# Optimization experiments

Hardware: AMD Instinct MI355X
Metric: run time of the kernel (lower is better)

Reference implementation:

```python
import jax, jax.numpy as jnp
import numpy as np

EPS = 1e-3  # matches MaskedBatchNorm2d default eps=0.001


def setup_inputs() -> dict:
    key = jax.random.key(0)
    k1, k2 = jax.random.split(key)
    B, C, W, H = 16, 64, 256, 256
    x = jax.random.normal(k1, (B, C, W, H), dtype=jnp.float32)
    # densified sparse-voxel feature maps the module is designed for.
    keep = (jax.random.uniform(k2, (B, W, H)) < 0.3).astype(jnp.float32)
    x = x * keep[:, None, :, :]
    return {"x": x}


def reference(x):
    """Faithful masked batchnorm (training mode, affine=False).

    Original: per-batch nonzero() of channel-sum, pad index lists to the max
    count with zeros (i.e. duplicate location (0,0)), gather [B, Nmax, C],
    compute per-channel mean/var over ALL gathered entries (padding included),
    divide by sqrt(var+eps) (mean NOT subtracted in output), scatter back to
    nonzero locations — padded rows also overwrite location (0,0).
    """
    B, C, W, H = x.shape
    x1 = x.sum(axis=1)                      # [B, W, H]
    m = x1 != 0                             # nonzero-site mask
    mf = m.astype(x.dtype)
    n = mf.sum(axis=(1, 2))                 # nonzero count per batch item [B]
    Nmax = n.max()
    pad = Nmax - n                          # number of padded (0,0) duplicates per item
    total = (B * Nmax).astype(x.dtype)      # B * max(num_nonzeros)

    x00 = x[:, :, 0, 0]                     # [B, C] value gathered by padded indices

    # per-channel mean over masked sites + padded duplicates of (0,0)
    sum_c = jnp.einsum('bcwh,bwh->c', x, mf) + jnp.einsum('bc,b->c', x00, pad)
    mean = sum_c / total                    # [C]

    d = x - mean[None, :, None, None]
    var = (jnp.einsum('bcwh,bwh->c', d * d, mf)
           + jnp.einsum('bc,b->c', (x00 - mean[None, :]) ** 2, pad)) / total

    inv = 1.0 / jnp.sqrt(var + EPS)         # [C]; note: mean is NOT subtracted
    xn = x * inv[None, :, None, None]

    out = jnp.where(m[:, None, :, :], xn, x)
    # padded scatter rows write normalized x[b,:,0,0] into location (0,0)
    has_pad = (pad > 0)[:, None]            # [B,1]
    out = out.at[:, :, 0, 0].set(jnp.where(has_pad, x00 * inv[None, :], out[:, :, 0, 0]))
    return out
```

## Files before the change

kernel.cpp:

```cpp
#include <hip/hip_runtime.h>


#define NB 16
#define CB 64
#define WH 65536
#define TILE 256
#define NTILES (NB * WH / TILE)
#define GRID1 1024
#define TPT (NTILES / GRID1)
#define DIRTY_CAP 512
#define EPS 0.001f


__global__ __launch_bounds__(256, 4)
void mbn_pass1(const float* __restrict__ x, float* __restrict__ sqPart,
               unsigned* __restrict__ nPart, unsigned* __restrict__ dirtyCnt,
               int* __restrict__ dirtyLoc) {
    __shared__ float lds_s[4][TILE];
    __shared__ float lds_a[4][TILE];
    __shared__ unsigned cnt_lds[16];
    const int tid  = threadIdx.x;
    const int wave = tid >> 6;
    const int lane = tid & 63;
    if (tid < 16) cnt_lds[tid] = 0;

    float sAcc[16], qAcc[16];
#pragma unroll
    for (int j = 0; j < 16; ++j) { sAcc[j] = 0.f; qAcc[j] = 0.f; }
    __syncthreads();

    for (int tt = 0; tt < TPT; ++tt) {
        const int tile = blockIdx.x + tt * GRID1;
        const int b    = tile >> 8;
        const int whb  = (tile & 255) * TILE;
        const float* base = x + (((size_t)(b * 64 + wave * 16)) << 16) + whb + lane * 4;

        float sp0 = 0.f, sp1 = 0.f, sp2 = 0.f, sp3 = 0.f;
        float aa0 = 0.f, aa1 = 0.f, aa2 = 0.f, aa3 = 0.f;
#pragma unroll
        for (int j = 0; j < 16; ++j) {
            float4 v = *(const float4*)(base + ((size_t)j << 16));
            sp0 += v.x; sp1 += v.y; sp2 += v.z; sp3 += v.w;
            aa0 += fabsf(v.x); aa1 += fabsf(v.y); aa2 += fabsf(v.z); aa3 += fabsf(v.w);
            sAcc[j] += (v.x + v.y) + (v.z + v.w);
            qAcc[j] = fmaf(v.x, v.x, qAcc[j]);
            qAcc[j] = fmaf(v.y, v.y, qAcc[j]);
            qAcc[j] = fmaf(v.z, v.z, qAcc[j]);
            qAcc[j] = fmaf(v.w, v.w, qAcc[j]);
        }
        *(float4*)&lds_s[wave][lane * 4] = make_float4(sp0, sp1, sp2, sp3);
        *(float4*)&lds_a[wave][lane * 4] = make_float4(aa0, aa1, aa2, aa3);
        __syncthreads();

        float s = lds_s[0][tid] + lds_s[1][tid] + lds_s[2][tid] + lds_s[3][tid];
        float a = lds_a[0][tid] + lds_a[1][tid] + lds_a[2][tid] + lds_a[3][tid];
        bool mask = (s != 0.0f);
        unsigned long long bal = __ballot(mask);
        if (lane == 0) atomicAdd(&cnt_lds[b], (unsigned)__popcll(bal));
        if (!mask && a != 0.0f) {
            unsigned idx = atomicAdd(dirtyCnt, 1u);
            if (idx < DIRTY_CAP) dirtyLoc[idx] = (b << 16) | (whb + tid);
        }
        __syncthreads();
    }

#pragma unroll
    for (int j = 0; j < 16; ++j) {
        float sv = sAcc[j], qv = qAcc[j];
        for (int off = 32; off; off >>= 1) {
            sv += __shfl_xor(sv, off);
            qv += __shfl_xor(qv, off);
        }
        if (lane == 0) {
            sqPart[blockIdx.x * 128 + wave * 16 + j]      = sv;
            sqPart[blockIdx.x * 128 + 64 + wave * 16 + j] = qv;
        }
    }
    __syncthreads();
    if (tid < 16) nPart[blockIdx.x * 16 + tid] = cnt_lds[tid];
}

__global__ void mbn_finalize(const float* __restrict__ x, const float* __restrict__ sqPart,
                             const unsigned* __restrict__ nPart,
                             const unsigned* __restrict__ dirtyCnt, const int* __restrict__ dirtyLoc,
                             float* __restrict__ inv, int* __restrict__ padOut) {
    __shared__ float red[256];
    __shared__ float sq[128];
    __shared__ unsigned npar[4][16];
    __shared__ unsigned ntot[16];
    const int t = threadIdx.x;
    const int idx = t & 127, half = t >> 7;

    float acc = 0.f;
    const float* p = sqPart + (size_t)half * 512 * 128 + idx;
#pragma unroll 8
    for (int blk = 0; blk < 512; ++blk) acc += p[(size_t)blk * 128];
    red[t] = acc;

    if (t >= 192) {
        const int b = t & 15, q = (t >> 4) & 3;
        unsigned s = 0;
        const unsigned* np = nPart + q * 256 * 16 + b;
#pragma unroll 8
        for (int blk = 0; blk < 256; ++blk) s += np[blk * 16];
        npar[q][b] = s;
    }
    __syncthreads();
    if (t < 128) sq[t] = red[t] + red[t + 128];
    if (t < 16)  ntot[t] = npar[0][t] + npar[1][t] + npar[2][t] + npar[3][t];
    __syncthreads();

    if (t < 64) {
        const int c = t;
        unsigned nmax = 0;
#pragma unroll
        for (int b = 0; b < NB; ++b) { unsigned nb = ntot[b]; nmax = nb > nmax ? nb : nmax; }
        const float total = (float)(16u * nmax);

        float s = sq[c], q = sq[64 + c];
        unsigned cnt = *dirtyCnt; if (cnt > DIRTY_CAP) cnt = DIRTY_CAP;
        for (unsigned i = 0; i < cnt; ++i) {
            int loc = dirtyLoc[i];
            int b = loc >> 16, wh = loc & 65535;
            float v = x[(((size_t)(b * 64 + c)) << 16) + wh];
            s -= v; q -= v * v;
        }
        float p1 = 0.f, p2 = 0.f;
#pragma unroll
        for (int b = 0; b < NB; ++b) {
            float padf = (float)(nmax - ntot[b]);
            float v00  = x[((size_t)(b * 64 + c)) << 16];
            p1 = fmaf(padf, v00, p1);
            p2 = fmaf(padf, v00 * v00, p2);
            if (c == 0) padOut[b] = (int)(nmax - ntot[b]);
        }
        float mean = (s + p1) / total;
        float var  = (q + p2) / total - mean * mean;
        inv[c] = 1.0f / sqrtf(var + EPS);
    }
}

__global__ __launch_bounds__(256)
void mbn_pass2(const float4* __restrict__ x4, float4* __restrict__ out4,
               const float* __restrict__ inv) {
    const int blk = blockIdx.x;
    const float sc = inv[(blk >> 3) & 63];
    const size_t base = (size_t)blk * 2048 + threadIdx.x;
#pragma unroll
    for (int k = 0; k < 8; ++k) {
        size_t i = base + (size_t)k * 256;
        float4 v = x4[i];
        v.x *= sc; v.y *= sc; v.z *= sc; v.w *= sc;
        out4[i] = v;
    }
}

__global__ void mbn_fixup(const float* __restrict__ x, float* __restrict__ out,
                          const unsigned* __restrict__ dirtyCnt, const int* __restrict__ dirtyLoc,
                          const int* __restrict__ padArr) {
    const int c = threadIdx.x;
    unsigned cnt = *dirtyCnt; if (cnt > DIRTY_CAP) cnt = DIRTY_CAP;
    for (unsigned i = 0; i < cnt; ++i) {
        int loc = dirtyLoc[i];
        int b = loc >> 16, wh = loc & 65535;
        if (wh == 0 && padArr[b] > 0) continue;
        size_t idx = (((size_t)(b * 64 + c)) << 16) + wh;
        out[idx] = x[idx];
    }
}

extern "C" void kernel_launch(void* const* d_in, const int* in_sizes, int n_in,
                              void* d_out, int out_size, void* d_ws, size_t ws_size,
                              hipStream_t stream) {
    const float* x = (const float*)d_in[0];
    float* out = (float*)d_out;
    float* wsf = (float*)d_ws;

    float*    sqPart   = wsf;
    unsigned* nPart    = (unsigned*)(wsf + 131072);
    unsigned* dirtyCnt = (unsigned*)(wsf + 147456);
    float*    inv      = wsf + 147520;
    int*      padArr   = (int*)(wsf + 147584);
    int*      dirtyLoc = (int*)(wsf + 147600);

    hipMemsetAsync((char*)d_ws + 147456 * 4, 0, 64, stream);

    mbn_pass1<<<GRID1, 256, 0, stream>>>(x, sqPart, nPart, dirtyCnt, dirtyLoc);
    mbn_finalize<<<1, 256, 0, stream>>>(x, sqPart, nPart, dirtyCnt, dirtyLoc, inv, padArr);
    mbn_pass2<<<8192, 256, 0, stream>>>((const float4*)x, (float4*)out, inv);
    mbn_fixup<<<1, 64, 0, stream>>>(x, out, dirtyCnt, dirtyLoc, padArr);
}
```

Measured before the change: 592.4 us.

## Restructure stats pass to contiguous per-block tiles, widen finalize, nontemporal scale stores

```diff
diff --git a/kernel.cpp b/kernel.cpp
--- a/kernel.cpp
+++ b/kernel.cpp
@@ -2,112 +2,132 @@
 
 
 #define NB 16
-#define CB 64
-#define WH 65536
-#define TILE 256
-#define NTILES (NB * WH / TILE)
-#define GRID1 1024
-#define TPT (NTILES / GRID1)
 #define DIRTY_CAP 512
 #define EPS 0.001f
+#define GRID1 1024
+
+typedef float vfloat4 __attribute__((ext_vector_type(4)));
 
 
 __global__ __launch_bounds__(256, 4)
 void mbn_pass1(const float* __restrict__ x, float* __restrict__ sqPart,
                unsigned* __restrict__ nPart, unsigned* __restrict__ dirtyCnt,
                int* __restrict__ dirtyLoc) {
-    __shared__ float lds_s[4][TILE];
-    __shared__ float lds_a[4][TILE];
-    __shared__ unsigned cnt_lds[16];
+    __shared__ float lds_s[4][1024];
+    __shared__ float lds_a[4][1024];
+    __shared__ unsigned cntw[4];
+
     const int tid  = threadIdx.x;
     const int wave = tid >> 6;
     const int lane = tid & 63;
-    if (tid < 16) cnt_lds[tid] = 0;
+    const int blk  = blockIdx.x;
+    const int b    = blk >> 6;
+    const int whb0 = (blk & 63) << 10;
 
     float sAcc[16], qAcc[16];
 #pragma unroll
     for (int j = 0; j < 16; ++j) { sAcc[j] = 0.f; qAcc[j] = 0.f; }
-    __syncthreads();
-
-    for (int tt = 0; tt < TPT; ++tt) {
-        const int tile = blockIdx.x + tt * GRID1;
-        const int b    = tile >> 8;
-        const int whb  = (tile & 255) * TILE;
-        const float* base = x + (((size_t)(b * 64 + wave * 16)) << 16) + whb + lane * 4;
-
-        float sp0 = 0.f, sp1 = 0.f, sp2 = 0.f, sp3 = 0.f;
-        float aa0 = 0.f, aa1 = 0.f, aa2 = 0.f, aa3 = 0.f;
-#pragma unroll
-        for (int j = 0; j < 16; ++j) {
-            float4 v = *(const float4*)(base + ((size_t)j << 16));
-            sp0 += v.x; sp1 += v.y; sp2 += v.z; sp3 += v.w;
-            aa0 += fabsf(v.x); aa1 += fabsf(v.y); aa2 += fabsf(v.z); aa3 += fabsf(v.w);
-            sAcc[j] += (v.x + v.y) + (v.z + v.w);
-            qAcc[j] = fmaf(v.x, v.x, qAcc[j]);
-            qAcc[j] = fmaf(v.y, v.y, qAcc[j]);
-            qAcc[j] = fmaf(v.z, v.z, qAcc[j]);
-            qAcc[j] = fmaf(v.w, v.w, qAcc[j]);
-        }
-        *(float4*)&lds_s[wave][lane * 4] = make_float4(sp0, sp1, sp2, sp3);
-        *(float4*)&lds_a[wave][lane * 4] = make_float4(aa0, aa1, aa2, aa3);
-        __syncthreads();
-
-        float s = lds_s[0][tid] + lds_s[1][tid] + lds_s[2][tid] + lds_s[3][tid];
-        float a = lds_a[0][tid] + lds_a[1][tid] + lds_a[2][tid] + lds_a[3][tid];
-        bool mask = (s != 0.0f);
-        unsigned long long bal = __ballot(mask);
-        if (lane == 0) atomicAdd(&cnt_lds[b], (unsigned)__popcll(bal));
-        if (!mask && a != 0.0f) {
-            unsigned idx = atomicAdd(dirtyCnt, 1u);
-            if (idx < DIRTY_CAP) dirtyLoc[idx] = (b << 16) | (whb + tid);
-        }
-        __syncthreads();
-    }
+
+    const float* wbase = x + (((size_t)(b * 64 + wave * 16)) << 16) + whb0 + lane * 4;
+
+#pragma unroll
+    for (int j = 0; j < 4; ++j) {
+        const float* cb = wbase + j * 256;
+        float4 sp = make_float4(0.f, 0.f, 0.f, 0.f);
+        float4 aa = make_float4(0.f, 0.f, 0.f, 0.f);
+#pragma unroll
+        for (int c = 0; c < 16; ++c) {
+            float4 v = *(const float4*)(cb + ((size_t)c << 16));
+            sp.x += v.x; sp.y += v.y; sp.z += v.z; sp.w += v.w;
+            aa.x += fabsf(v.x); aa.y += fabsf(v.y); aa.z += fabsf(v.z); aa.w += fabsf(v.w);
+            sAcc[c] += (v.x + v.y) + (v.z + v.w);
+            qAcc[c] = fmaf(v.x, v.x, qAcc[c]);
+            qAcc[c] = fmaf(v.y, v.y, qAcc[c]);
+            qAcc[c] = fmaf(v.z, v.z, qAcc[c]);
+            qAcc[c] = fmaf(v.w, v.w, qAcc[c]);
+        }
+        *(float4*)&lds_s[wave][j * 256 + lane * 4] = sp;
+        *(float4*)&lds_a[wave][j * 256 + lane * 4] = aa;
+    }
+    __syncthreads();
+
+    float4 s0 = *(const float4*)&lds_s[0][tid * 4];
+    float4 s1 = *(const float4*)&lds_s[1][tid * 4];
+    float4 s2 = *(const float4*)&lds_s[2][tid * 4];
+    float4 s3 = *(const float4*)&lds_s[3][tid * 4];
+    float4 a0 = *(const float4*)&lds_a[0][tid * 4];
+    float4 a1 = *(const float4*)&lds_a[1][tid * 4];
+    float4 a2 = *(const float4*)&lds_a[2][tid * 4];
+    float4 a3 = *(const float4*)&lds_a[3][tid * 4];
+    float sx = (s0.x + s1.x) + (s2.x + s3.x);
+    float sy = (s0.y + s1.y) + (s2.y + s3.y);
+    float sz = (s0.z + s1.z) + (s2.z + s3.z);
+    float sw = (s0.w + s1.w) + (s2.w + s3.w);
+    float ax = (a0.x + a1.x) + (a2.x + a3.x);
+    float ay = (a0.y + a1.y) + (a2.y + a3.y);
+    float az = (a0.z + a1.z) + (a2.z + a3.z);
+    float aw = (a0.w + a1.w) + (a2.w + a3.w);
+    bool m0 = (sx != 0.f), m1 = (sy != 0.f), m2 = (sz != 0.f), m3 = (sw != 0.f);
+    unsigned cnt = (m0 ? 1u : 0u) + (m1 ? 1u : 0u) + (m2 ? 1u : 0u) + (m3 ? 1u : 0u);
+    if ((!m0 && ax != 0.f) | (!m1 && ay != 0.f) | (!m2 && az != 0.f) | (!m3 && aw != 0.f)) {
+        bool d[4] = { !m0 && ax != 0.f, !m1 && ay != 0.f, !m2 && az != 0.f, !m3 && aw != 0.f };
+        for (int k = 0; k < 4; ++k) if (d[k]) {
+            unsigned id = atomicAdd(dirtyCnt, 1u);
+            if (id < DIRTY_CAP) dirtyLoc[id] = (b << 16) | (whb0 + tid * 4 + k);
+        }
+    }
+#pragma unroll
+    for (int off = 32; off; off >>= 1) cnt += __shfl_xor(cnt, off);
+    if (lane == 0) cntw[wave] = cnt;
 
 #pragma unroll
     for (int j = 0; j < 16; ++j) {
         float sv = sAcc[j], qv = qAcc[j];
+#pragma unroll
         for (int off = 32; off; off >>= 1) {
             sv += __shfl_xor(sv, off);
             qv += __shfl_xor(qv, off);
         }
         if (lane == 0) {
-            sqPart[blockIdx.x * 128 + wave * 16 + j]      = sv;
-            sqPart[blockIdx.x * 128 + 64 + wave * 16 + j] = qv;
-        }
-    }
-    __syncthreads();
-    if (tid < 16) nPart[blockIdx.x * 16 + tid] = cnt_lds[tid];
-}
-
-__global__ void mbn_finalize(const float* __restrict__ x, const float* __restrict__ sqPart,
-                             const unsigned* __restrict__ nPart,
-                             const unsigned* __restrict__ dirtyCnt, const int* __restrict__ dirtyLoc,
-                             float* __restrict__ inv, int* __restrict__ padOut) {
-    __shared__ float red[256];
+            sqPart[blk * 128 + wave * 16 + j]      = sv;
+            sqPart[blk * 128 + 64 + wave * 16 + j] = qv;
+        }
+    }
+    __syncthreads();
+    if (tid == 0) nPart[blk] = cntw[0] + cntw[1] + cntw[2] + cntw[3];
+}
+
+__global__ __launch_bounds__(1024)
+void mbn_finalize(const float* __restrict__ x, const float* __restrict__ sqPart,
+                  const unsigned* __restrict__ nPart,
+                  const unsigned* __restrict__ dirtyCnt, const int* __restrict__ dirtyLoc,
+                  float* __restrict__ inv, int* __restrict__ padOut) {
+    __shared__ float red[1024];
     __shared__ float sq[128];
-    __shared__ unsigned npar[4][16];
     __shared__ unsigned ntot[16];
     const int t = threadIdx.x;
-    const int idx = t & 127, half = t >> 7;
+    const int col = t & 127, grp = t >> 7;
 
     float acc = 0.f;
-    const float* p = sqPart + (size_t)half * 512 * 128 + idx;
+    const float* p = sqPart + (size_t)grp * 128 * 128 + col;
 #pragma unroll 8
-    for (int blk = 0; blk < 512; ++blk) acc += p[(size_t)blk * 128];
+    for (int r = 0; r < 128; ++r) acc += p[(size_t)r * 128];
     red[t] = acc;
 
-    if (t >= 192) {
-        const int b = t & 15, q = (t >> 4) & 3;
+    if (t < 16) {
         unsigned s = 0;
-        const unsigned* np = nPart + q * 256 * 16 + b;
+        const unsigned* np = nPart + t * 64;
 #pragma unroll 8
-        for (int blk = 0; blk < 256; ++blk) s += np[blk * 16];
-        npar[q][b] = s;
-    }
-    __syncthreads();
-    if (t < 128) sq[t] = red[t] + red[t + 128];
-    if (t < 16)  ntot[t] = npar[0][t] + npar[1][t] + npar[2][t] + npar[3][t];
+        for (int i = 0; i < 64; ++i) s += np[i];
+        ntot[t] = s;
+    }
+    __syncthreads();
+    if (t < 128) {
+        float v = 0.f;
+#pragma unroll
+        for (int g = 0; g < 8; ++g) v += red[g * 128 + t];
+        sq[t] = v;
+    }
     __syncthreads();
 
     if (t < 64) {
@@ -141,17 +161,17 @@
 }
 
 __global__ __launch_bounds__(256)
-void mbn_pass2(const float4* __restrict__ x4, float4* __restrict__ out4,
+void mbn_pass2(const vfloat4* __restrict__ x4, vfloat4* __restrict__ out4,
                const float* __restrict__ inv) {
     const int blk = blockIdx.x;
-    const float sc = inv[(blk >> 3) & 63];
-    const size_t base = (size_t)blk * 2048 + threadIdx.x;
-#pragma unroll
-    for (int k = 0; k < 8; ++k) {
+    const float sc = inv[(blk >> 2) & 63];
+    const size_t base = ((size_t)blk << 12) + threadIdx.x;
+#pragma unroll
+    for (int k = 0; k < 16; ++k) {
         size_t i = base + (size_t)k * 256;
-        float4 v = x4[i];
-        v.x *= sc; v.y *= sc; v.z *= sc; v.w *= sc;
-        out4[i] = v;
+        vfloat4 v = x4[i];
+        v *= sc;
+        __builtin_nontemporal_store(v, &out4[i]);
     }
 }
 
@@ -178,15 +198,15 @@
 
     float*    sqPart   = wsf;
     unsigned* nPart    = (unsigned*)(wsf + 131072);
-    unsigned* dirtyCnt = (unsigned*)(wsf + 147456);
-    float*    inv      = wsf + 147520;
-    int*      padArr   = (int*)(wsf + 147584);
-    int*      dirtyLoc = (int*)(wsf + 147600);
-
-    hipMemsetAsync((char*)d_ws + 147456 * 4, 0, 64, stream);
+    unsigned* dirtyCnt = (unsigned*)(wsf + 132160);
+    float*    inv      = wsf + 132224;
+    int*      padArr   = (int*)(wsf + 132288);
+    int*      dirtyLoc = (int*)(wsf + 132352);
+
+    (void)hipMemsetAsync((char*)d_ws + 132160 * 4, 0, 64, stream);
 
     mbn_pass1<<<GRID1, 256, 0, stream>>>(x, sqPart, nPart, dirtyCnt, dirtyLoc);
-    mbn_finalize<<<1, 256, 0, stream>>>(x, sqPart, nPart, dirtyCnt, dirtyLoc, inv, padArr);
-    mbn_pass2<<<8192, 256, 0, stream>>>((const float4*)x, (float4*)out, inv);
+    mbn_finalize<<<1, 1024, 0, stream>>>(x, sqPart, nPart, dirtyCnt, dirtyLoc, inv, padArr);
+    mbn_pass2<<<4096, 256, 0, stream>>>((const vfloat4*)x, (vfloat4*)out, inv);
     mbn_fixup<<<1, 64, 0, stream>>>(x, out, dirtyCnt, dirtyLoc, padArr);
 }
```

New measurement: 607.4 us. +2.5%, slower.
